# Kernel optimization log

Measured on AMD Instinct MI355X. Metric: run time of the kernel, lower is better.

The kernel has to match this reference:

```python
import jax, jax.numpy as jnp
import numpy as np

B, TGT, SRC, DIM = 8, 1024, 1024, 1024

def setup_inputs() -> dict:
    key = jax.random.key(0)
    k1, k2, k3, k4, k5 = jax.random.split(key, 5)
    s = 1.0 / np.sqrt(DIM)
    return {
        "input": jax.random.normal(k1, (B, TGT, DIM), dtype=jnp.float32),
        "context": jax.random.normal(k2, (B, SRC, DIM), dtype=jnp.float32),
        "context_lengths": jax.random.randint(k3, (B,), 1, SRC + 1, dtype=jnp.int64 if jax.config.jax_enable_x64 else jnp.int32),
        "W_in": jax.random.normal(k4, (DIM, DIM), dtype=jnp.float32) * s,   # torch Linear weight [out,in]
        "W_out": jax.random.normal(k5, (DIM, 2 * DIM), dtype=jnp.float32) * s,
    }

def reference(input, context, context_lengths, W_in, W_out):
    # GlobalAttention, attn_type='general', include_rnn=True, dropout=0 (identity)
    # score: (W_in @ h_t) . h_s  -> [B, TGT, SRC]
    h_t = jnp.einsum('btd,ed->bte', input, W_in)
    align = jnp.einsum('bte,bse->bts', h_t, context)
    # mask positions >= length with -inf before softmax over source dim
    mask = jnp.arange(align.shape[-1])[None, :] < context_lengths[:, None]  # [B, SRC]
    align = jnp.where(mask[:, None, :], align, -jnp.inf)
    align_vectors = jax.nn.softmax(align, axis=-1)                         # [B, TGT, SRC]
    c = jnp.einsum('bts,bsd->btd', align_vectors, context)                 # context vector
    concat = jnp.concatenate([c, input], axis=-1)                          # [B, TGT, 2*DIM]
    attn_h = jnp.tanh(jnp.einsum('btf,df->btd', concat, W_out))            # linear_out (no bias) + tanh
    return attn_h, align_vectors
```

## Files before the change

kernel.cpp:

```cpp
#include <hip/hip_runtime.h>

typedef __attribute__((ext_vector_type(8))) short short8;
typedef __attribute__((ext_vector_type(4))) float f32x4;

#define DIM  1024
#define BT   8192
#define NBAT 8
#define KSOFF (1 << 29)

__device__ __forceinline__ unsigned short f2bf(float x){
  union { float f; unsigned u; } un; un.f = x;
  unsigned r = un.u + 0x7fffu + ((un.u >> 16) & 1u);
  return (unsigned short)(r >> 16);
}
__device__ __forceinline__ float bf2f(unsigned short h){
  union { unsigned u; float f; } un; un.u = ((unsigned)h) << 16;
  return un.f;
}

__global__ void prep_kernel(const float* __restrict__ in,
                            unsigned short* __restrict__ in_hi,
                            unsigned short* __restrict__ in_lo,
                            const float* __restrict__ Win,
                            unsigned short* __restrict__ wi_hi,
                            unsigned short* __restrict__ wi_lo,
                            const float* __restrict__ Wout,
                            unsigned short* __restrict__ wo_hi){
  const int N0 = (BT * DIM) >> 2;
  const int N1 = N0 + ((DIM * DIM) >> 2);
  const int N2 = N1 + ((DIM * 2 * DIM) >> 2);
  int stride = gridDim.x * blockDim.x;
  for (int i = blockIdx.x * blockDim.x + threadIdx.x; i < N2; i += stride){
    if (i < N0){
      float4 v = ((const float4*)in)[i];
      ushort4 h, l;
      h.x = f2bf(v.x); l.x = f2bf(v.x - bf2f(h.x));
      h.y = f2bf(v.y); l.y = f2bf(v.y - bf2f(h.y));
      h.z = f2bf(v.z); l.z = f2bf(v.z - bf2f(h.z));
      h.w = f2bf(v.w); l.w = f2bf(v.w - bf2f(h.w));
      ((ushort4*)in_hi)[i] = h;
      ((ushort4*)in_lo)[i] = l;
    } else if (i < N1){
      int j = i - N0;
      float4 v = ((const float4*)Win)[j];
      ushort4 h, l;
      h.x = f2bf(v.x); l.x = f2bf(v.x - bf2f(h.x));
      h.y = f2bf(v.y); l.y = f2bf(v.y - bf2f(h.y));
      h.z = f2bf(v.z); l.z = f2bf(v.z - bf2f(h.z));
      h.w = f2bf(v.w); l.w = f2bf(v.w - bf2f(h.w));
      ((ushort4*)wi_hi)[j] = h;
      ((ushort4*)wi_lo)[j] = l;
    } else {
      int j = i - N1;
      float4 v = ((const float4*)Wout)[j];
      ushort4 h;
      h.x = f2bf(v.x); h.y = f2bf(v.y); h.z = f2bf(v.z); h.w = f2bf(v.w);
      ((ushort4*)wo_hi)[j] = h;
    }
  }
}

__global__ void ctx_prep_kernel(const float* __restrict__ ctx,
                                unsigned short* __restrict__ hi,
                                unsigned short* __restrict__ lo,
                                unsigned short* __restrict__ ctxT){
  __shared__ unsigned short t[64][65];
  int bz = blockIdx.z;
  int s0 = blockIdx.x << 6, d0 = blockIdx.y << 6;
  int tx = threadIdx.x, ty = threadIdx.y;
  const size_t base = (((size_t)bz << 10) + s0) * DIM + d0;
  const float* src = ctx + base;
  unsigned short* hrow = hi + base;
  unsigned short* lrow = lo + base;
  #pragma unroll
  for (int i = ty; i < 64; i += 4){
    float v = src[(size_t)i * DIM + tx];
    unsigned short h = f2bf(v);
    hrow[(size_t)i * DIM + tx] = h;
    lrow[(size_t)i * DIM + tx] = f2bf(v - bf2f(h));
    t[i][tx] = h;
  }
  __syncthreads();
  unsigned short* dst = ctxT + (((size_t)bz << 10) + d0) * DIM + s0;
  #pragma unroll
  for (int i = ty; i < 64; i += 4)
    dst[(size_t)i * DIM + tx] = t[tx][i];
}

__global__ __launch_bounds__(256) void softmax_kernel(float* __restrict__ sc,
                                                      unsigned short* __restrict__ Pb,
                                                      const int* __restrict__ lens){
  const int row = blockIdx.x;
  const int len = lens[row >> 10];
  const int tid = threadIdx.x;
  const int lane = tid & 63, wid = tid >> 6;
  float* rp = sc + ((size_t)row << 10);
  const int s0 = tid << 2;
  float4 v;
  if (s0 < len) v = ((const float4*)rp)[tid];
  else          v = (float4){0.f, 0.f, 0.f, 0.f};
  float x0 = (s0 + 0 < len) ? v.x : -INFINITY;
  float x1 = (s0 + 1 < len) ? v.y : -INFINITY;
  float x2 = (s0 + 2 < len) ? v.z : -INFINITY;
  float x3 = (s0 + 3 < len) ? v.w : -INFINITY;
  float wmax = fmaxf(fmaxf(x0, x1), fmaxf(x2, x3));
  #pragma unroll
  for (int o = 32; o > 0; o >>= 1) wmax = fmaxf(wmax, __shfl_xor(wmax, o));
  __shared__ float red[8];
  if (lane == 0) red[wid] = wmax;
  __syncthreads();
  float mx = fmaxf(fmaxf(red[0], red[1]), fmaxf(red[2], red[3]));
  float e0 = (s0 + 0 < len) ? __expf(x0 - mx) : 0.f;
  float e1 = (s0 + 1 < len) ? __expf(x1 - mx) : 0.f;
  float e2 = (s0 + 2 < len) ? __expf(x2 - mx) : 0.f;
  float e3 = (s0 + 3 < len) ? __expf(x3 - mx) : 0.f;
  float ws = e0 + e1 + e2 + e3;
  #pragma unroll
  for (int o = 32; o > 0; o >>= 1) ws += __shfl_xor(ws, o);
  if (lane == 0) red[4 + wid] = ws;
  __syncthreads();
  float inv = 1.f / (red[4] + red[5] + red[6] + red[7]);
  float4 p; p.x = e0 * inv; p.y = e1 * inv; p.z = e2 * inv; p.w = e3 * inv;
  ((float4*)rp)[tid] = p;
  ushort4 pb; pb.x = f2bf(p.x); pb.y = f2bf(p.y); pb.z = f2bf(p.z); pb.w = f2bf(p.w);
  ((ushort4*)(Pb + ((size_t)row << 10)))[tid] = pb;
}

__device__ __forceinline__ int lds_off(int r, int kb){
  return r * 64 + (((kb ^ ((r >> 1) & 3))) << 4);
}

__device__ __forceinline__ void gld16(void* lds, const void* g){
  __builtin_amdgcn_global_load_lds(
      (__attribute__((address_space(1))) void*)(g),
      (__attribute__((address_space(3))) void*)(lds), 16, 0, 0);
}

template<bool SPLIT, int EPI, int KSPLIT>
__global__ __launch_bounds__(256, 2) void gemm_kernel(
    const unsigned short* __restrict__ Ah,  const unsigned short* __restrict__ Al,
    const unsigned short* __restrict__ Ah2, const unsigned short* __restrict__ Al2,
    const unsigned short* __restrict__ Bh,  const unsigned short* __restrict__ Bl,
    int K, int lda, int ldb,
    long long aStride, long long bStride, long long oStride,
    float* __restrict__ outF, unsigned short* __restrict__ o1,
    unsigned short* __restrict__ o2, int ldo,
    const int* __restrict__ lens, int lmode)
{
  constexpr int TILE = 128 * 64;
  __shared__ __align__(16) char smem[(SPLIT ? 4 : 2) * TILE];
  char* sAh = smem;
  char* sBh = smem + TILE;
  char* sAl = smem + (SPLIT ? 2 : 0) * TILE;
  char* sBl = smem + (SPLIT ? 3 : 0) * TILE;

  const int tid  = threadIdx.x;
  const int lane = tid & 63;
  const int wid  = tid >> 6;
  const int z    = blockIdx.z;

  int bx = blockIdx.x, by = blockIdx.y;
  if (gridDim.x == 8 && gridDim.y == 8){
    int o = bx + (by << 3);
    int k = o & 7, j = o >> 3;
    bx = ((k & 3) << 1) | (j & 1);  by = ((k >> 2) << 2) | (j >> 1);
  } else if (gridDim.x == 8 && (gridDim.y & 7) == 0){
    int o = bx + (by << 3);
    int xcd = o & 7, j = o >> 3;
    bx = j & 7;
    by = xcd * (gridDim.y >> 3) + (j >> 3);
  }
  const int m0 = by * 128;
  const int n0 = bx * 128;

  int Keff = K;
  if (lmode){
    const int len = lens[z];
    if (lmode == 1 && n0 >= len) return;
    if (lmode == 2){
      int kc = (len + 31) & ~31;
      Keff = kc < K ? kc : K;
    }
  }

  const unsigned short* gAh  = Ah  + (size_t)z * aStride + (size_t)m0 * lda;
  const unsigned short* gAh2 = Ah2 + (size_t)z * aStride + (size_t)m0 * lda;
  const unsigned short* gBh  = Bh  + (size_t)z * bStride + (size_t)n0 * ldb;
  const unsigned short* gAl  = SPLIT ? (Al  + (size_t)z * aStride + (size_t)m0 * lda) : (const unsigned short*)0;
  const unsigned short* gAl2 = SPLIT ? (Al2 + (size_t)z * aStride + (size_t)m0 * lda) : (const unsigned short*)0;
  const unsigned short* gBl  = SPLIT ? (Bl  + (size_t)z * bStride + (size_t)n0 * ldb) : (const unsigned short*)0;

  const int rS0 = (wid << 5) + (lane >> 2);
  const int rS1 = rS0 + 16;
  const int cS0 = ((lane & 3) ^ ((rS0 >> 1) & 3)) << 3;
  const int cS1 = ((lane & 3) ^ ((rS1 >> 1) & 3)) << 3;
  const int dS0 = (wid << 5) << 6;
  const int dS1 = dS0 + (16 << 6);
  const unsigned short* qAh0  = gAh  + (size_t)rS0 * lda + cS0;
  const unsigned short* qAh1  = gAh  + (size_t)rS1 * lda + cS1;
  const unsigned short* qAh20 = gAh2 + (size_t)rS0 * lda + cS0;
  const unsigned short* qAh21 = gAh2 + (size_t)rS1 * lda + cS1;
  const unsigned short* qBh0  = gBh  + (size_t)rS0 * ldb + cS0;
  const unsigned short* qBh1  = gBh  + (size_t)rS1 * ldb + cS1;
  const unsigned short* qAl0  = SPLIT ? (gAl  + (size_t)rS0 * lda + cS0) : (const unsigned short*)0;
  const unsigned short* qAl1  = SPLIT ? (gAl  + (size_t)rS1 * lda + cS1) : (const unsigned short*)0;
  const unsigned short* qAl20 = SPLIT ? (gAl2 + (size_t)rS0 * lda + cS0) : (const unsigned short*)0;
  const unsigned short* qAl21 = SPLIT ? (gAl2 + (size_t)rS1 * lda + cS1) : (const unsigned short*)0;
  const unsigned short* qBl0  = SPLIT ? (gBl  + (size_t)rS0 * ldb + cS0) : (const unsigned short*)0;
  const unsigned short* qBl1  = SPLIT ? (gBl  + (size_t)rS1 * ldb + cS1) : (const unsigned short*)0;

  f32x4 acc[4][4];
  #pragma unroll
  for (int m = 0; m < 4; m++)
    #pragma unroll
    for (int n = 0; n < 4; n++)
      acc[m][n] = (f32x4){0.f, 0.f, 0.f, 0.f};

  const int wr = (wid >> 1) * 64;
  const int wc = (wid & 1) * 64;
  const int fr = lane & 15;
  const int kb = lane >> 4;

  for (int k0 = 0; k0 < Keff; k0 += 32){
    __syncthreads();
    const unsigned short *a0, *a1, *l0 = 0, *l1 = 0;
    if (KSPLIT != KSOFF && k0 >= KSPLIT){
      int q = k0 - KSPLIT;
      a0 = qAh20 + q; a1 = qAh21 + q;
      if (SPLIT){ l0 = qAl20 + q; l1 = qAl21 + q; }
    } else {
      a0 = qAh0 + k0; a1 = qAh1 + k0;
      if (SPLIT){ l0 = qAl0 + k0; l1 = qAl1 + k0; }
    }
    gld16(sAh + dS0, a0);
    gld16(sAh + dS1, a1);
    gld16(sBh + dS0, qBh0 + k0);
    gld16(sBh + dS1, qBh1 + k0);
    if (SPLIT){
      gld16(sAl + dS0, l0);
      gld16(sAl + dS1, l1);
      gld16(sBl + dS0, qBl0 + k0);
      gld16(sBl + dS1, qBl1 + k0);
    }
    __syncthreads();

    short8 ah[4], bh[4], al[4], bl[4];
    #pragma unroll
    for (int m = 0; m < 4; m++){
      int off = lds_off(wr + m * 16 + fr, kb);
      ah[m] = *(const short8*)(sAh + off);
      if (SPLIT) al[m] = *(const short8*)(sAl + off);
    }
    #pragma unroll
    for (int n = 0; n < 4; n++){
      int off = lds_off(wc + n * 16 + fr, kb);
      bh[n] = *(const short8*)(sBh + off);
      if (SPLIT) bl[n] = *(const short8*)(sBl + off);
    }
    #pragma unroll
    for (int m = 0; m < 4; m++)
      #pragma unroll
      for (int n = 0; n < 4; n++){
        acc[m][n] = __builtin_amdgcn_mfma_f32_16x16x32_bf16(ah[m], bh[n], acc[m][n], 0, 0, 0);
        if (SPLIT){
          acc[m][n] = __builtin_amdgcn_mfma_f32_16x16x32_bf16(ah[m], bl[n], acc[m][n], 0, 0, 0);
          acc[m][n] = __builtin_amdgcn_mfma_f32_16x16x32_bf16(al[m], bh[n], acc[m][n], 0, 0, 0);
        }
      }
  }

  const int rbase = (lane >> 4) * 2 * 2;
  const int cbase = lane & 15;
  #pragma unroll
  for (int m = 0; m < 4; m++){
    #pragma unroll
    for (int n = 0; n < 4; n++){
      f32x4 v = acc[m][n];
      int col = n0 + wc + n * 16 + cbase;
      #pragma unroll
      for (int j = 0; j < 4; j++){
        int row = m0 + wr + m * 16 + rbase + j;
        float val = v[j];
        size_t idx = (size_t)row * ldo + col;
        if (EPI == 0){
          unsigned short h = f2bf(val);
          o1[(size_t)z * oStride + idx] = h;
          o2[(size_t)z * oStride + idx] = f2bf(val - bf2f(h));
        } else if (EPI == 1){
          outF[(size_t)z * oStride + idx] = val;
        } else if (EPI == 4){
          o1[(size_t)z * oStride + idx] = f2bf(val);
        } else {
          outF[idx] = tanhf(val);
        }
      }
    }
  }
}

template<int EPI, int NT, int KSPLIT>
__global__ __launch_bounds__(256, 2) void gemm_pipe128_kernel(
    const unsigned short* __restrict__ Ah, const unsigned short* __restrict__ Ah2,
    const unsigned short* __restrict__ Bh,
    int lda, int ldb,
    float* __restrict__ outF, unsigned short* __restrict__ o1, int ldo)
{
  constexpr int TA  = 8192;
  constexpr int OFF_B = TA;
  constexpr int BUF = 2 * TA;

  __shared__ __align__(16) char sm0[BUF];
  __shared__ __align__(16) char sm1[BUF];
  __shared__ __align__(16) char sm2[BUF];

  const int tid  = threadIdx.x;
  const int lane = tid & 63;
  const int w    = tid >> 6;

  int bx = blockIdx.x, by = blockIdx.y;
  {
    int o = bx + (by << 3);
    int xcd = o & 7, j = o >> 3;
    bx = j & 7;
    by = xcd * (gridDim.y >> 3) + (j >> 3);
  }
  const int m0 = by << 7;
  const int n0 = bx << 7;

  const unsigned short* gAh  = Ah  + (size_t)m0 * lda;
  const unsigned short* gAh2 = Ah2 + (size_t)m0 * lda;
  const unsigned short* gBh  = Bh  + (size_t)n0 * ldb;

  const int rS0 = (w << 5) + (lane >> 2);
  const int rS1 = rS0 + 16;
  const int cS0 = ((lane & 3) ^ ((rS0 >> 1) & 3)) << 3;
  const int cS1 = ((lane & 3) ^ ((rS1 >> 1) & 3)) << 3;
  const unsigned short* pA0  = gAh  + (size_t)rS0 * lda + cS0;
  const unsigned short* pA1  = gAh  + (size_t)rS1 * lda + cS1;
  const unsigned short* pA20 = gAh2 + (size_t)rS0 * lda + cS0;
  const unsigned short* pA21 = gAh2 + (size_t)rS1 * lda + cS1;
  const unsigned short* pB0  = gBh  + (size_t)rS0 * ldb + cS0;
  const unsigned short* pB1  = gBh  + (size_t)rS1 * ldb + cS1;
  const int dS0 = (w << 5) << 6;
  const int dS1 = dS0 + (16 << 6);

  f32x4 acc[4][4];
  #pragma unroll
  for (int m = 0; m < 4; m++)
    #pragma unroll
    for (int n = 0; n < 4; n++)
      acc[m][n] = (f32x4){0.f, 0.f, 0.f, 0.f};

  const int wr = (w >> 1) << 6;
  const int wc = (w & 1) << 6;
  const int fr = lane & 15;
  const int kb = lane >> 4;

  short8 ah, bh[4];

#define STAGE(WR, KS) do { int _k = (KS);                                   \
    const unsigned short *_s0, *_s1;                                        \
    if (_k >= KSPLIT){ int _q = _k - KSPLIT; _s0 = pA20 + _q; _s1 = pA21 + _q; } \
    else             { _s0 = pA0 + _k;       _s1 = pA1 + _k; }              \
    gld16(WR + dS0, _s0);                                                   \
    gld16(WR + dS1, _s1);                                                   \
    gld16(WR + OFF_B + dS0, pB0 + _k);                                      \
    gld16(WR + OFF_B + dS1, pB1 + _k);                                      \
  } while(0)

#define READS_B(RD) do {                                                    \
    _Pragma("unroll")                                                       \
    for (int n = 0; n < 4; n++)                                             \
      bh[n] = *(const short8*)((RD) + OFF_B + lds_off(wc + n * 16 + fr, kb)); \
  } while(0)

#define READS_A(RD, M)                                                      \
    ah = *(const short8*)((RD) + lds_off(wr + (M) * 16 + fr, kb))

#define MFMA_M(M) do {                                                      \
    __builtin_amdgcn_s_setprio(1);                                          \
    _Pragma("unroll")                                                       \
    for (int n = 0; n < 4; n++)                                             \
      acc[M][n] = __builtin_amdgcn_mfma_f32_16x16x32_bf16(ah, bh[n], acc[M][n], 0, 0, 0); \
    __builtin_amdgcn_s_setprio(0);                                          \
  } while(0)

#define BAR() do { __builtin_amdgcn_s_barrier();                            \
                   asm volatile("" ::: "memory"); } while(0)
#define LGKM0() asm volatile("s_waitcnt lgkmcnt(0)" ::: "memory")
#define VMCNT4() asm volatile("s_waitcnt vmcnt(4)" ::: "memory")

#define STEP(RD, WR, T) do {                                                \
    int _ks = (((T) + 2 < NT) ? (T) + 2 : NT - 1) << 5;   \
    READS_B(RD); READS_A(RD, 0);                                            \
    STAGE(WR, _ks);                                                         \
    BAR(); LGKM0(); MFMA_M(0); BAR();                                       \
    READS_A(RD, 1);                                                        \
    BAR(); LGKM0(); MFMA_M(1); BAR();                                       \
    READS_A(RD, 2);                                                        \
    BAR(); LGKM0(); MFMA_M(2); BAR();                                       \
    READS_A(RD, 3);                                                        \
    BAR(); LGKM0(); MFMA_M(3);                                              \
    VMCNT4();                                                               \
    BAR();                                                                  \
  } while(0)

  STAGE(sm0, 0);
  STAGE(sm1, 32);
  VMCNT4();
  BAR();

  for (int t = 0; t < NT; t += 3){
    STEP(sm0, sm2, t);
    if (t + 1 < NT) STEP(sm1, sm0, t + 1);
    if (t + 2 < NT) STEP(sm2, sm1, t + 2);
  }
#undef STAGE
#undef READS_B
#undef READS_A
#undef MFMA_M
#undef BAR
#undef LGKM0
#undef VMCNT4
#undef STEP

  const int rbase = (lane >> 4) << 2;
  const int cbase = lane & 15;
  #pragma unroll
  for (int m = 0; m < 4; m++){
    #pragma unroll
    for (int n = 0; n < 4; n++){
      f32x4 v = acc[m][n];
      int col = n0 + wc + n * 16 + cbase;
      #pragma unroll
      for (int j = 0; j < 4; j++){
        int row = m0 + wr + m * 16 + rbase + j;
        float val = v[j];
        size_t idx = (size_t)row * ldo + col;
        if (EPI == 3) outF[idx] = tanhf(val);
        else          o1[idx] = f2bf(val);
      }
    }
  }
}

extern "C" void kernel_launch(void* const* d_in, const int* in_sizes, int n_in,
                              void* d_out, int out_size, void* d_ws, size_t ws_size,
                              hipStream_t stream){
  const float* input   = (const float*)d_in[0];
  const float* context = (const float*)d_in[1];
  const int*   lens    = (const int*)d_in[2];
  const float* Win     = (const float*)d_in[3];
  const float* Wout    = (const float*)d_in[4];
  float* attn  = (float*)d_out;
  float* align = attn + (size_t)BT * DIM;

  char* ws = (char*)d_ws;
  size_t off = 0;
  auto alloc = [&](size_t bytes) -> char* {
    char* p = ws + off; off += (bytes + 255) & ~(size_t)255; return p;
  };
  const size_t MTD = (size_t)BT * DIM;
  unsigned short* in_hi = (unsigned short*)alloc(MTD * 2);
  unsigned short* in_lo = (unsigned short*)alloc(MTD * 2);
  unsigned short* cx_hi = (unsigned short*)alloc(MTD * 2);
  unsigned short* cx_lo = (unsigned short*)alloc(MTD * 2);
  unsigned short* wi_hi = (unsigned short*)alloc((size_t)DIM * DIM * 2);
  unsigned short* wi_lo = (unsigned short*)alloc((size_t)DIM * DIM * 2);
  unsigned short* ht_hi = (unsigned short*)alloc(MTD * 2);
  unsigned short* ht_lo = (unsigned short*)alloc(MTD * 2);
  unsigned short* cxT   = (unsigned short*)alloc(MTD * 2);
  unsigned short* c_hi  = (unsigned short*)alloc(MTD * 2);
  unsigned short* wo_hi = (unsigned short*)alloc((size_t)DIM * 2 * DIM * 2);
  unsigned short* p_bf  = cx_hi;
  if (off > ws_size) return;

  prep_kernel<<<4096, 256, 0, stream>>>(input, in_hi, in_lo,
                                        Win, wi_hi, wi_lo, Wout, wo_hi);
  ctx_prep_kernel<<<dim3(16, 16, NBAT), dim3(64, 4), 0, stream>>>(context, cx_hi, cx_lo, cxT);

  gemm_kernel<true, 0, KSOFF><<<dim3(8, 64, 1), 256, 0, stream>>>(
      in_hi, in_lo, in_hi, in_lo, wi_hi, wi_lo, DIM, DIM, DIM,
      0, 0, 0,
      nullptr, ht_hi, ht_lo, DIM, nullptr, 0);
  gemm_kernel<true, 1, KSOFF><<<dim3(8, 8, NBAT), 256, 0, stream>>>(
      ht_hi, ht_lo, ht_hi, ht_lo, cx_hi, cx_lo, DIM, DIM, DIM,
      (long long)DIM * 1024, (long long)DIM * 1024, (long long)DIM * 1024,
      align, nullptr, nullptr, DIM, lens, 1);
  softmax_kernel<<<BT, 256, 0, stream>>>(align, p_bf, lens);
  gemm_kernel<false, 4, KSOFF><<<dim3(8, 8, NBAT), 256, 0, stream>>>(
      p_bf, nullptr, p_bf, nullptr, cxT, nullptr, DIM, DIM, DIM,
      (long long)DIM * 1024, (long long)DIM * 1024, (long long)1024 * 1024,
      nullptr, c_hi, nullptr, DIM, lens, 2);
  gemm_pipe128_kernel<3, 64, 1024><<<dim3(8, 64), 256, 0, stream>>>(
      c_hi, in_hi, wo_hi, DIM, 2 * DIM,
      attn, nullptr, DIM);
}
```

Baseline: 223.5 us.

## Replace triple-buffered K32 pipeline with double-buffered K64 steps in output GEMM

The final output-projection GEMM changes from a three-stage ring of 32-wide K tiles to two 64-wide K buffers. Each step now stages the next 64-wide tile, computes two halves with one barrier per step, and waits with vmcnt(0). This removes the many per-row-block barriers and lgkm waits of the old scheme, which add synchronisation overhead. In exchange, load latency is hidden by only one buffer of lookahead, and LDS use per block rises from 48KB to 64KB.

```diff
diff --git a/kernel.cpp b/kernel.cpp
--- a/kernel.cpp
+++ b/kernel.cpp
@@ -299,19 +299,18 @@
 }
 
 template<int EPI, int NT, int KSPLIT>
-__global__ __launch_bounds__(256, 2) void gemm_pipe128_kernel(
+__global__ __launch_bounds__(256, 2) void gemm_dbuf64_kernel(
     const unsigned short* __restrict__ Ah, const unsigned short* __restrict__ Ah2,
     const unsigned short* __restrict__ Bh,
     int lda, int ldb,
     float* __restrict__ outF, unsigned short* __restrict__ o1, int ldo)
 {
-  constexpr int TA  = 8192;
-  constexpr int OFF_B = TA;
-  constexpr int BUF = 2 * TA;
+  constexpr int SUB   = 8192;
+  constexpr int OFF_B = 2 * SUB;
+  constexpr int BUF   = 4 * SUB;
 
   __shared__ __align__(16) char sm0[BUF];
   __shared__ __align__(16) char sm1[BUF];
-  __shared__ __align__(16) char sm2[BUF];
 
   const int tid  = threadIdx.x;
   const int lane = tid & 63;
@@ -356,73 +355,61 @@
   const int fr = lane & 15;
   const int kb = lane >> 4;
 
-  short8 ah, bh[4];
-
-#define STAGE(WR, KS) do { int _k = (KS);                                   \
+#define STAGE_H(WR, H, KE) do { int _k = (KE);                              \
     const unsigned short *_s0, *_s1;                                        \
     if (_k >= KSPLIT){ int _q = _k - KSPLIT; _s0 = pA20 + _q; _s1 = pA21 + _q; } \
     else             { _s0 = pA0 + _k;       _s1 = pA1 + _k; }              \
-    gld16(WR + dS0, _s0);                                                   \
-    gld16(WR + dS1, _s1);                                                   \
-    gld16(WR + OFF_B + dS0, pB0 + _k);                                      \
-    gld16(WR + OFF_B + dS1, pB1 + _k);                                      \
+    gld16(WR + (H) * SUB + dS0, _s0);                                       \
+    gld16(WR + (H) * SUB + dS1, _s1);                                       \
+    gld16(WR + OFF_B + (H) * SUB + dS0, pB0 + _k);                          \
+    gld16(WR + OFF_B + (H) * SUB + dS1, pB1 + _k);                          \
   } while(0)
 
-#define READS_B(RD) do {                                                    \
+#define STAGE64(WR, T1) do {                                                \
+    STAGE_H(WR, 0, (T1) * 64);                                              \
+    STAGE_H(WR, 1, (T1) * 64 + 32);                                         \
+  } while(0)
+
+#define HALF(RD, H) do {                                                    \
+    short8 bh[4], ah;                                                       \
     _Pragma("unroll")                                                       \
     for (int n = 0; n < 4; n++)                                             \
-      bh[n] = *(const short8*)((RD) + OFF_B + lds_off(wc + n * 16 + fr, kb)); \
-  } while(0)
-
-#define READS_A(RD, M)                                                      \
-    ah = *(const short8*)((RD) + lds_off(wr + (M) * 16 + fr, kb))
-
-#define MFMA_M(M) do {                                                      \
-    __builtin_amdgcn_s_setprio(1);                                          \
+      bh[n] = *(const short8*)((RD) + OFF_B + (H) * SUB + lds_off(wc + n * 16 + fr, kb)); \
     _Pragma("unroll")                                                       \
-    for (int n = 0; n < 4; n++)                                             \
-      acc[M][n] = __builtin_amdgcn_mfma_f32_16x16x32_bf16(ah, bh[n], acc[M][n], 0, 0, 0); \
-    __builtin_amdgcn_s_setprio(0);                                          \
+    for (int m = 0; m < 4; m++){                                            \
+      ah = *(const short8*)((RD) + (H) * SUB + lds_off(wr + m * 16 + fr, kb)); \
+      __builtin_amdgcn_s_setprio(1);                                        \
+      _Pragma("unroll")                                                     \
+      for (int n = 0; n < 4; n++)                                           \
+        acc[m][n] = __builtin_amdgcn_mfma_f32_16x16x32_bf16(ah, bh[n], acc[m][n], 0, 0, 0); \
+      __builtin_amdgcn_s_setprio(0);                                        \
+    }                                                                       \
   } while(0)
 
 #define BAR() do { __builtin_amdgcn_s_barrier();                            \
                    asm volatile("" ::: "memory"); } while(0)
-#define LGKM0() asm volatile("s_waitcnt lgkmcnt(0)" ::: "memory")
-#define VMCNT4() asm volatile("s_waitcnt vmcnt(4)" ::: "memory")
-
-#define STEP(RD, WR, T) do {                                                \
-    int _ks = (((T) + 2 < NT) ? (T) + 2 : NT - 1) << 5;   \
-    READS_B(RD); READS_A(RD, 0);                                            \
-    STAGE(WR, _ks);                                                         \
-    BAR(); LGKM0(); MFMA_M(0); BAR();                                       \
-    READS_A(RD, 1);                                                        \
-    BAR(); LGKM0(); MFMA_M(1); BAR();                                       \
-    READS_A(RD, 2);                                                        \
-    BAR(); LGKM0(); MFMA_M(2); BAR();                                       \
-    READS_A(RD, 3);                                                        \
-    BAR(); LGKM0(); MFMA_M(3);                                              \
-    VMCNT4();                                                               \
+
+#define STEP64(RD, WR, T) do {                                              \
+    if ((T) + 1 < NT) STAGE64(WR, (T) + 1);                                 \
+    HALF(RD, 0);                                                            \
+    HALF(RD, 1);                                                            \
+    asm volatile("s_waitcnt vmcnt(0)" ::: "memory");                        \
     BAR();                                                                  \
   } while(0)
 
-  STAGE(sm0, 0);
-  STAGE(sm1, 32);
-  VMCNT4();
+  STAGE64(sm0, 0);
+  asm volatile("s_waitcnt vmcnt(0)" ::: "memory");
   BAR();
 
-  for (int t = 0; t < NT; t += 3){
-    STEP(sm0, sm2, t);
-    if (t + 1 < NT) STEP(sm1, sm0, t + 1);
-    if (t + 2 < NT) STEP(sm2, sm1, t + 2);
-  }
-#undef STAGE
-#undef READS_B
-#undef READS_A
-#undef MFMA_M
+  for (int t = 0; t < NT; t += 2){
+    STEP64(sm0, sm1, t);
+    STEP64(sm1, sm0, t + 1);
+  }
+#undef STAGE_H
+#undef STAGE64
+#undef HALF
 #undef BAR
-#undef LGKM0
-#undef VMCNT4
-#undef STEP
+#undef STEP64
 
   const int rbase = (lane >> 4) << 2;
   const int cbase = lane & 15;
@@ -492,7 +479,7 @@
       p_bf, nullptr, p_bf, nullptr, cxT, nullptr, DIM, DIM, DIM,
       (long long)DIM * 1024, (long long)DIM * 1024, (long long)1024 * 1024,
       nullptr, c_hi, nullptr, DIM, lens, 2);
-  gemm_pipe128_kernel<3, 64, 1024><<<dim3(8, 64), 256, 0, stream>>>(
+  gemm_dbuf64_kernel<3, 32, 1024><<<dim3(8, 64), 256, 0, stream>>>(
       c_hi, in_hi, wo_hi, DIM, 2 * DIM,
       attn, nullptr, DIM);
 }
```

New measurement: 225.3 us. No clear change (+0.8%).
